# Performance work log

Hardware: AMD Instinct MI355X
Metric: run time of the kernel (lower is better)

The kernel has to match this reference:

```python
import jax, jax.numpy as jnp
import numpy as np

N_NODES = 50000
N_EDGES = 800000
D = 64
D_OUT = 64


def setup_inputs() -> dict:
    key = jax.random.key(0)
    ks = jax.random.split(key, 7)
    h_src = jax.random.normal(ks[0], (N_NODES, D), dtype=jnp.float32)
    h_dst = jax.random.normal(ks[1], (N_NODES, D), dtype=jnp.float32)
    e = jax.random.normal(ks[2], (N_EDGES, D), dtype=jnp.float32)
    src = jax.random.randint(ks[3], (N_EDGES,), 0, N_NODES, dtype=jnp.int32)
    dst = jax.random.randint(ks[4], (N_EDGES,), 0, N_NODES, dtype=jnp.int32)
    W = jax.random.normal(ks[5], (D_OUT, 2 * D), dtype=jnp.float32) * 0.05  # nn.Linear weight [out, in]
    b = jax.random.normal(ks[6], (D_OUT,), dtype=jnp.float32) * 0.05
    return {"h_src": h_src, "h_dst": h_dst, "e": e, "src": src, "dst": dst, "W": W, "b": b}


def reference(h_src, h_dst, e, src, dst, W, b):
    # u_dot_e: per-edge dot product between gathered src features and edge features
    h_u = h_src[src]                                   # [E, D] gather
    score = jnp.sum(h_u * e, axis=-1)                  # [E]
    exp_s = jnp.exp(score)                             # raw exp, as in original (no max-subtract)
    # segment-sum exp over dst nodes, then edge-wise normalize (edge softmax)
    denom = jax.ops.segment_sum(exp_s, dst, num_segments=N_NODES)  # [N]
    pi = exp_s / denom[dst]                            # [E]
    # weighted neighbor aggregation: sum_e pi * h_src[src] into dst
    msg = h_u * pi[:, None]                            # [E, D]
    h_sum = jax.ops.segment_sum(msg, dst, num_segments=N_NODES)    # [N, D]
    # concat self features with aggregated neighbors, then linear
    h_total = jnp.concatenate([h_dst, h_sum], axis=1)  # [N, 2D]
    return h_total @ W.T + b                           # [N, D_OUT]
```

## Files before the change

kernel.cpp:

```cpp
#include <hip/hip_runtime.h>

#define N_NODES 50000
#define N_EDGES 800000
#define D 64
#define CAP 64

typedef float vf4 __attribute__((ext_vector_type(4)));

__global__ __launch_bounds__(256) void k1_score(
    const vf4* __restrict__ h_src4, const vf4* __restrict__ e4,
    const int* __restrict__ src, const int* __restrict__ dst,
    int* __restrict__ count, int2* __restrict__ slots) {
    int t = threadIdx.x;
    int edge = blockIdx.x * 32 + (t >> 3);
    int l8 = t & 7;
    int s = src[edge];
    const vf4* hp = h_src4 + (size_t)s * 16;
    const vf4* ep = e4 + (size_t)edge * 16;
    vf4 u0 = hp[l8];
    vf4 u1 = hp[8 + l8];
    vf4 e0 = __builtin_nontemporal_load(ep + l8);
    vf4 e1 = __builtin_nontemporal_load(ep + 8 + l8);
    float v = u0[0]*e0[0] + u0[1]*e0[1] + u0[2]*e0[2] + u0[3]*e0[3]
            + u1[0]*e1[0] + u1[1]*e1[1] + u1[2]*e1[2] + u1[3]*e1[3];
    v += __shfl_xor(v, 1);
    v += __shfl_xor(v, 2);
    v += __shfl_xor(v, 4);
    if (l8 == 0) {
        float ex = expf(v);
        int d = dst[edge];
        int pos = atomicAdd(&count[d], 1);
        if (pos < CAP)
            slots[(size_t)d * CAP + pos] = make_int2(s, __float_as_int(ex));
    }
}

__global__ __launch_bounds__(256) void k2k3(
    const vf4* __restrict__ h_src4, const vf4* __restrict__ h_dst4,
    const int* __restrict__ count, const int2* __restrict__ slots,
    const float* __restrict__ W, const float* __restrict__ b,
    float* __restrict__ out) {
    __shared__ float Wl[128 * 64];
    __shared__ __align__(16) float ht[16][128];
    int t = threadIdx.x;
    for (int i = t; i < 128 * 64; i += 256) {
        int o = i >> 7, k = i & 127;
        Wl[k * 64 + o] = W[i];
    }
    int node0 = blockIdx.x * 16;
    int n = t >> 4;
    int l16 = t & 15;
    int node = node0 + n;
    int cnt = count[node];
    cnt = cnt < CAP ? cnt : CAP;
    const int2* row = slots + (size_t)node * CAP;
    vf4 acc = {0.f, 0.f, 0.f, 0.f};
    float dsum = 0.f;
    for (int base = 0; base < cnt; base += 16) {
        int rem = cnt - base;
        int2 se = make_int2(0, 0);
        if (l16 < rem) se = row[base + l16];
        #pragma unroll
        for (int j = 0; j < 16; ++j) {
            int   sj = __shfl(se.x, j, 16);
            float wj = __int_as_float(__shfl(se.y, j, 16));
            vf4   gj = h_src4[(size_t)sj * 16 + l16];
            acc += wj * gj;
            dsum += wj;
        }
    }
    float inv = (cnt > 0) ? 1.f / dsum : 0.f;
    acc *= inv;
    vf4 hd = h_dst4[(size_t)node * 16 + l16];
    ((vf4*)&ht[n][0])[l16] = hd;
    ((vf4*)&ht[n][64])[l16] = acc;
    __syncthreads();

    int o = t & 63;
    int g = t >> 6;
    float bias = b[o];
    float a0 = bias, a1 = bias, a2 = bias, a3 = bias;
    const float* h0 = &ht[g * 4 + 0][0];
    const float* h1 = &ht[g * 4 + 1][0];
    const float* h2 = &ht[g * 4 + 2][0];
    const float* h3 = &ht[g * 4 + 3][0];
    #pragma unroll
    for (int k = 0; k < 128; k += 4) {
        float w0 = Wl[(k + 0) * 64 + o];
        float w1 = Wl[(k + 1) * 64 + o];
        float w2 = Wl[(k + 2) * 64 + o];
        float w3 = Wl[(k + 3) * 64 + o];
        vf4 p0 = *(const vf4*)&h0[k];
        vf4 p1 = *(const vf4*)&h1[k];
        vf4 p2 = *(const vf4*)&h2[k];
        vf4 p3 = *(const vf4*)&h3[k];
        a0 += p0[0]*w0 + p0[1]*w1 + p0[2]*w2 + p0[3]*w3;
        a1 += p1[0]*w0 + p1[1]*w1 + p1[2]*w2 + p1[3]*w3;
        a2 += p2[0]*w0 + p2[1]*w1 + p2[2]*w2 + p2[3]*w3;
        a3 += p3[0]*w0 + p3[1]*w1 + p3[2]*w2 + p3[3]*w3;
    }
    out[(size_t)(node0 + g * 4 + 0) * 64 + o] = a0;
    out[(size_t)(node0 + g * 4 + 1) * 64 + o] = a1;
    out[(size_t)(node0 + g * 4 + 2) * 64 + o] = a2;
    out[(size_t)(node0 + g * 4 + 3) * 64 + o] = a3;
}

extern "C" void kernel_launch(void* const* d_in, const int* in_sizes, int n_in,
                              void* d_out, int out_size, void* d_ws, size_t ws_size,
                              hipStream_t stream) {
    const float* h_src = (const float*)d_in[0];
    const float* h_dst = (const float*)d_in[1];
    const float* e     = (const float*)d_in[2];
    const int*   src   = (const int*)d_in[3];
    const int*   dst   = (const int*)d_in[4];
    const float* W     = (const float*)d_in[5];
    const float* b     = (const float*)d_in[6];
    float* out = (float*)d_out;

    auto align256 = [](size_t x) { return (x + 255) & ~(size_t)255; };
    char* ws = (char*)d_ws;
    int*  count = (int*)ws;
    int2* slots = (int2*)(ws + align256((size_t)N_NODES * 4));

    hipMemsetAsync(count, 0, (size_t)N_NODES * 4, stream);

    k1_score<<<N_EDGES / 32, 256, 0, stream>>>(
        (const vf4*)h_src, (const vf4*)e, src, dst, count, slots);
    k2k3<<<N_NODES / 16, 256, 0, stream>>>(
        (const vf4*)h_src, (const vf4*)h_dst, count, slots, W, b, out);
}
```

Baseline: 403.3 us.

## Move edge score computation from bucketing kernel into per-node aggregation kernel

The first kernel now only buckets edges by destination and stores (src, edge id) pairs. The score dot product and exp move into the aggregation kernel, which gathers h_src once per edge and reuses that row for both the score and the weighted message. This removes the second h_src gather, but the edge feature rows are now read through a random gather by edge id instead of a coalesced streaming load, and a 16-lane shuffle reduction is added per edge. The edge batch per iteration also drops from 16 to 8.

```diff
diff --git a/kernel.cpp b/kernel.cpp
--- a/kernel.cpp
+++ b/kernel.cpp
@@ -7,36 +7,20 @@
 
 typedef float vf4 __attribute__((ext_vector_type(4)));
 
-__global__ __launch_bounds__(256) void k1_score(
-    const vf4* __restrict__ h_src4, const vf4* __restrict__ e4,
+__global__ __launch_bounds__(256) void k1_bucket(
     const int* __restrict__ src, const int* __restrict__ dst,
     int* __restrict__ count, int2* __restrict__ slots) {
-    int t = threadIdx.x;
-    int edge = blockIdx.x * 32 + (t >> 3);
-    int l8 = t & 7;
-    int s = src[edge];
-    const vf4* hp = h_src4 + (size_t)s * 16;
-    const vf4* ep = e4 + (size_t)edge * 16;
-    vf4 u0 = hp[l8];
-    vf4 u1 = hp[8 + l8];
-    vf4 e0 = __builtin_nontemporal_load(ep + l8);
-    vf4 e1 = __builtin_nontemporal_load(ep + 8 + l8);
-    float v = u0[0]*e0[0] + u0[1]*e0[1] + u0[2]*e0[2] + u0[3]*e0[3]
-            + u1[0]*e1[0] + u1[1]*e1[1] + u1[2]*e1[2] + u1[3]*e1[3];
-    v += __shfl_xor(v, 1);
-    v += __shfl_xor(v, 2);
-    v += __shfl_xor(v, 4);
-    if (l8 == 0) {
-        float ex = expf(v);
-        int d = dst[edge];
-        int pos = atomicAdd(&count[d], 1);
-        if (pos < CAP)
-            slots[(size_t)d * CAP + pos] = make_int2(s, __float_as_int(ex));
-    }
+    int i = blockIdx.x * 256 + threadIdx.x;
+    int s = src[i];
+    int d = dst[i];
+    int pos = atomicAdd(&count[d], 1);
+    if (pos < CAP)
+        slots[(size_t)d * CAP + pos] = make_int2(s, i);
 }
 
 __global__ __launch_bounds__(256) void k2k3(
     const vf4* __restrict__ h_src4, const vf4* __restrict__ h_dst4,
+    const vf4* __restrict__ e4,
     const int* __restrict__ count, const int2* __restrict__ slots,
     const float* __restrict__ W, const float* __restrict__ b,
     float* __restrict__ out) {
@@ -56,17 +40,24 @@
     const int2* row = slots + (size_t)node * CAP;
     vf4 acc = {0.f, 0.f, 0.f, 0.f};
     float dsum = 0.f;
-    for (int base = 0; base < cnt; base += 16) {
-        int rem = cnt - base;
+    for (int base = 0; base < cnt; base += 8) {
         int2 se = make_int2(0, 0);
-        if (l16 < rem) se = row[base + l16];
+        if (l16 < 8 && base + l16 < cnt) se = row[base + l16];
         #pragma unroll
-        for (int j = 0; j < 16; ++j) {
-            int   sj = __shfl(se.x, j, 16);
-            float wj = __int_as_float(__shfl(se.y, j, 16));
-            vf4   gj = h_src4[(size_t)sj * 16 + l16];
-            acc += wj * gj;
-            dsum += wj;
+        for (int j = 0; j < 8; ++j) {
+            int sj = __shfl(se.x, j, 16);
+            int ej = __shfl(se.y, j, 16);
+            vf4 u  = h_src4[(size_t)sj * 16 + l16];
+            vf4 ev = e4[(size_t)ej * 16 + l16];
+            float p = u[0]*ev[0] + u[1]*ev[1] + u[2]*ev[2] + u[3]*ev[3];
+            p += __shfl_xor(p, 1, 16);
+            p += __shfl_xor(p, 2, 16);
+            p += __shfl_xor(p, 4, 16);
+            p += __shfl_xor(p, 8, 16);
+            float w = expf(p);
+            w = (base + j < cnt) ? w : 0.f;
+            acc += w * u;
+            dsum += w;
         }
     }
     float inv = (cnt > 0) ? 1.f / dsum : 0.f;
@@ -124,8 +115,8 @@
 
     hipMemsetAsync(count, 0, (size_t)N_NODES * 4, stream);
 
-    k1_score<<<N_EDGES / 32, 256, 0, stream>>>(
-        (const vf4*)h_src, (const vf4*)e, src, dst, count, slots);
+    k1_bucket<<<N_EDGES / 256, 256, 0, stream>>>(src, dst, count, slots);
     k2k3<<<N_NODES / 16, 256, 0, stream>>>(
-        (const vf4*)h_src, (const vf4*)h_dst, count, slots, W, b, out);
+        (const vf4*)h_src, (const vf4*)h_dst, (const vf4*)e,
+        count, slots, W, b, out);
 }
```

Measured after the change: 399.5 us. Within noise of the previous version (-0.9%).
